# Kernel tuning notes

Measured on AMD Instinct MI355X. Metric: run time of the kernel, lower is better.

Reference implementation:

```python
import jax, jax.numpy as jnp
import numpy as np

V, H, NH, I, L, P = 32000, 1024, 16, 4096, 8, 2048
B, S = 2, 2048
DH = H // NH
EPS = 1e-5


def setup_inputs() -> dict:
    key = jax.random.key(0)
    ks = jax.random.split(key, 12)
    std = 0.02
    inp = {
        'input_ids': jax.random.randint(ks[0], (B, S), 0, V),
        'attention_mask': jnp.ones((B, S), dtype=jnp.float32),
        'tok_emb': jax.random.normal(ks[1], (V, H), jnp.float32) * std,
        'pos_emb': jax.random.normal(ks[2], (P, H), jnp.float32) * std,
        # per-layer params stacked on leading L dim (torch Linear convention: y = x @ W.T + b)
        'Wq': jax.random.normal(ks[3], (L, H, H), jnp.float32) * std,
        'bq': jnp.zeros((L, H), jnp.float32),
        'Wk': jax.random.normal(ks[4], (L, H, H), jnp.float32) * std,
        'bk': jnp.zeros((L, H), jnp.float32),
        'Wv': jax.random.normal(ks[5], (L, H, H), jnp.float32) * std,
        'bv': jnp.zeros((L, H), jnp.float32),
        'Wi': jax.random.normal(ks[6], (L, I, H), jnp.float32) * std,
        'bi': jnp.zeros((L, I), jnp.float32),
        'Wo': jax.random.normal(ks[7], (L, H, I), jnp.float32) * std,
        'bo': jnp.zeros((L, H), jnp.float32),
        'ln1_g': jnp.ones((L, H), jnp.float32),
        'ln1_b': jnp.zeros((L, H), jnp.float32),
        'ln2_g': jnp.ones((L, H), jnp.float32),
        'ln2_b': jnp.zeros((L, H), jnp.float32),
        'lnf_g': jnp.ones((H,), jnp.float32),
        'lnf_b': jnp.zeros((H,), jnp.float32),
        'Wlm': jax.random.normal(ks[8], (V, H), jnp.float32) * std,
    }
    return inp


def _layer_norm(x, g, b):
    m = jnp.mean(x, axis=-1, keepdims=True)
    v = jnp.var(x, axis=-1, keepdims=True)
    return (x - m) * jax.lax.rsqrt(v + EPS) * g + b


def reference(input_ids, attention_mask, tok_emb, pos_emb, Wq, bq, Wk, bk, Wv, bv,
              Wi, bi, Wo, bo, ln1_g, ln1_b, ln2_g, ln2_b, lnf_g, lnf_b, Wlm):
    b, s = input_ids.shape
    h = tok_emb[input_ids] + pos_emb[jnp.arange(s)][None, :, :]  # [B,S,H]
    mask = (1.0 - attention_mask)[:, None, None, :] * -10000.0   # [B,1,1,S]
    scale = 1.0 / (DH ** 0.5)

    def split_heads(x):  # [B,S,H] -> [B,NH,S,DH]
        return x.reshape(b, s, NH, DH).transpose(0, 2, 1, 3)

    def block(h, p):
        wq, bq_, wk, bk_, wv, bv_, wi, bi_, wo, bo_, g1, b1, g2, b2 = p
        q = split_heads(h @ wq.T + bq_)
        k = split_heads(h @ wk.T + bk_)
        v = split_heads(h @ wv.T + bv_)
        scores = jnp.einsum('bhqd,bhkd->bhqk', q, k) * scale + mask
        probs = jax.nn.softmax(scores, axis=-1)
        ctx = jnp.einsum('bhqk,bhkd->bhqd', probs, v)
        ctx = ctx.transpose(0, 2, 1, 3).reshape(b, s, H)
        h1 = _layer_norm(h + ctx, g1, b1)
        mlp = jax.nn.gelu(h1 @ wi.T + bi_, approximate=False) @ wo.T + bo_
        return _layer_norm(h1 + mlp, g2, b2), None

    h, _ = jax.lax.scan(block, h, (Wq, bq, Wk, bk, Wv, bv, Wi, bi, Wo, bo,
                                   ln1_g, ln1_b, ln2_g, ln2_b))
    h = _layer_norm(h, lnf_g, lnf_b)
    return h @ Wlm.T  # [B,S,V]
```

## Files before the change

### kernel.cpp

```cpp
#include <hip/hip_runtime.h>
#include <hip/hip_bf16.h>

#define V_ 32000
#define H_ 1024
#define NH_ 16
#define I_ 4096
#define L_ 8
#define B_ 2
#define S_ 2048
#define DH_ 64
#define M_ 4096
#define QS_ 3072
#define NSP_ 2

typedef __attribute__((ext_vector_type(4))) float f32x4;
typedef __attribute__((ext_vector_type(8))) short s16x8;

#define BARRIER() do { asm volatile("" ::: "memory"); __builtin_amdgcn_s_barrier(); asm volatile("" ::: "memory"); } while (0)
#define SCHEDB()  __builtin_amdgcn_sched_barrier(0)

__device__ __forceinline__ unsigned short f2b(float f) {
  union { float f; unsigned u; } x; x.f = f;
  return (unsigned short)((x.u + 0x7FFFu + ((x.u >> 16) & 1u)) >> 16);
}

__device__ __forceinline__ void gl_lds16(const unsigned short* g, unsigned short* l) {
  __builtin_amdgcn_global_load_lds(
      (__attribute__((address_space(1))) const void*)g,
      (__attribute__((address_space(3))) void*)l, 16, 0, 0);
}

__global__ __launch_bounds__(256) void wcvt(const float* __restrict__ src,
                                            unsigned short* __restrict__ dst) {
  size_t i = ((size_t)blockIdx.x * 256 + threadIdx.x) * 4;
  float4 v = *(const float4*)(src + i);
  ushort4 b;
  b.x = f2b(v.x); b.y = f2b(v.y); b.z = f2b(v.z); b.w = f2b(v.w);
  *(ushort4*)(dst + i) = b;
}

__global__ __launch_bounds__(256) void qkvcat_all(const float* __restrict__ q,
                                                  const float* __restrict__ k,
                                                  const float* __restrict__ v,
                                                  unsigned short* __restrict__ dst) {
  size_t i = ((size_t)blockIdx.x * 256 + threadIdx.x) * 4;
  size_t l = i / (3u * H_ * H_);
  size_t r = i - l * (3u * H_ * H_);
  const float* s; size_t off;
  if (r < (size_t)H_ * H_)          { s = q; off = l * H_ * H_ + r; }
  else if (r < 2u * H_ * H_)        { s = k; off = l * H_ * H_ + r - (size_t)H_ * H_; }
  else                              { s = v; off = l * H_ * H_ + r - 2u * H_ * H_; }
  float4 vv = *(const float4*)(s + off);
  ushort4 b;
  b.x = f2b(vv.x); b.y = f2b(vv.y); b.z = f2b(vv.z); b.w = f2b(vv.w);
  *(ushort4*)(dst + i) = b;
}

__global__ __launch_bounds__(256) void qkvcat(const float* __restrict__ q,
                                              const float* __restrict__ k,
                                              const float* __restrict__ v,
                                              unsigned short* __restrict__ dst) {
  int i = (blockIdx.x * 256 + threadIdx.x) * 4;
  const float* s; int off;
  if (i < H_ * H_)          { s = q; off = i; }
  else if (i < 2 * H_ * H_) { s = k; off = i - H_ * H_; }
  else                      { s = v; off = i - 2 * H_ * H_; }
  float4 vv = *(const float4*)(s + off);
  ushort4 b;
  b.x = f2b(vv.x); b.y = f2b(vv.y); b.z = f2b(vv.z); b.w = f2b(vv.w);
  *(ushort4*)(dst + i) = b;
}

__global__ __launch_bounds__(256) void bcat(const float* __restrict__ bq,
                                            const float* __restrict__ bk,
                                            const float* __restrict__ bv,
                                            float* __restrict__ dst) {
  int i = blockIdx.x * 256 + threadIdx.x;
  int l = i / (3 * H_), r = i - l * 3 * H_;
  int p = r >> 10, c = r & (H_ - 1);
  const float* s = (p == 0) ? bq : ((p == 1) ? bk : bv);
  dst[i] = s[l * H_ + c];
}

__global__ __launch_bounds__(256) void embed_kernel(
    const int* __restrict__ ids, const float* __restrict__ tok,
    const float* __restrict__ pos, float* __restrict__ h,
    unsigned short* __restrict__ xbf)
{
  int row = blockIdx.x;
  int c4 = threadIdx.x;
  int id = ids[row];
  int s = row & (S_ - 1);
  float4 tv = ((const float4*)(tok + (size_t)id * H_))[c4];
  float4 pv = ((const float4*)(pos + (size_t)s * H_))[c4];
  float4 v; v.x = tv.x + pv.x; v.y = tv.y + pv.y; v.z = tv.z + pv.z; v.w = tv.w + pv.w;
  ((float4*)(h + (size_t)row * H_))[c4] = v;
  ushort4 b; b.x = f2b(v.x); b.y = f2b(v.y); b.z = f2b(v.z); b.w = f2b(v.w);
  ((ushort4*)(xbf + (size_t)row * H_))[c4] = b;
}

template<int EPI>
__global__ __launch_bounds__(256) void gemm_bt(
    const unsigned short* __restrict__ A, const unsigned short* __restrict__ Wb,
    const float* __restrict__ bias, float* __restrict__ outf,
    unsigned short* __restrict__ outb, unsigned short* __restrict__ vt,
    int M, int N, int K, int ksz)
{
  __shared__ unsigned short As[2][128][32];
  __shared__ unsigned short Bs[2][128][32];
  int t = threadIdx.x;
  int lane = t & 63, wid = t >> 6;
  int m0 = blockIdx.x * 128, n0 = blockIdx.y * 128;
  int z = blockIdx.z;
  int koff = z * ksz;
  const float* bz = (z == 0) ? bias : nullptr;
  if (EPI == 0) outf += (size_t)z * M * N;
  int wm = (wid >> 1) * 64, wn = (wid & 1) * 64;
  int fr = lane & 15, hi = lane >> 4;
  int lrow = lane >> 2;
  int lcolsw = (((lane & 3) ^ (lrow & 3)) * 8);
  int ke = ((hi ^ (fr & 3)) * 8);

  f32x4 acc[4][4] = {};

  const unsigned short* Abase = A  + (size_t)(m0 + wid * 32 + lrow) * K + lcolsw;
  const unsigned short* Bbase = Wb + (size_t)(n0 + wid * 32 + lrow) * K + lcolsw;

  auto stage = [&](int s, int k0) {
    gl_lds16(Abase + k0,                  &As[s][wid * 32][0]);
    gl_lds16(Abase + k0 + (size_t)16 * K, &As[s][wid * 32 + 16][0]);
    gl_lds16(Bbase + k0,                  &Bs[s][wid * 32][0]);
    gl_lds16(Bbase + k0 + (size_t)16 * K, &Bs[s][wid * 32 + 16][0]);
  };

  stage(0, koff);

  int cur = 0;
  for (int k0 = koff; k0 < koff + ksz; k0 += 32) {
    asm volatile("s_waitcnt vmcnt(0)" ::: "memory");
    BARRIER();
    if (k0 + 32 < koff + ksz) stage(cur ^ 1, k0 + 32);
    SCHEDB();
    s16x8 af[4], bfr[4];
    #pragma unroll
    for (int i = 0; i < 4; ++i) af[i]  = *(const s16x8*)(&As[cur][wm + i * 16 + fr][ke]);
    #pragma unroll
    for (int j = 0; j < 4; ++j) bfr[j] = *(const s16x8*)(&Bs[cur][wn + j * 16 + fr][ke]);
    #pragma unroll
    for (int i = 0; i < 4; ++i)
      #pragma unroll
      for (int j = 0; j < 4; ++j)
        acc[i][j] = __builtin_amdgcn_mfma_f32_16x16x32_bf16(af[i], bfr[j], acc[i][j], 0, 0, 0);
    cur ^= 1;
  }

  int fq = lane >> 4;
  if (EPI == 3) {
    #pragma unroll
    for (int i = 0; i < 4; ++i) {
      #pragma unroll
      for (int j = 0; j < 4; ++j) {
        int col = n0 + wn + j * 16 + fr;
        int row0_ = m0 + wm + i * 16 + fq * 4;
        float bcol = bz ? bz[col] : 0.f;
        if (col < 2 * H_) {
          #pragma unroll
          for (int r = 0; r < 4; ++r)
            outb[(size_t)(row0_ + r) * N + col] = f2b(acc[i][j][r] + bcol);
        } else {
          int d = col - 2 * H_;
          int bh = (row0_ >> 11) * NH_ + (d >> 6);
          int s0 = row0_ & (S_ - 1);
          ushort4 pk;
          pk.x = f2b(acc[i][j][0] + bcol);
          pk.y = f2b(acc[i][j][1] + bcol);
          pk.z = f2b(acc[i][j][2] + bcol);
          pk.w = f2b(acc[i][j][3] + bcol);
          *(ushort4*)(vt + ((size_t)bh * DH_ + (d & 63)) * S_ + s0) = pk;
        }
      }
    }
    return;
  }
  #pragma unroll
  for (int i = 0; i < 4; ++i) {
    #pragma unroll
    for (int j = 0; j < 4; ++j) {
      #pragma unroll
      for (int r = 0; r < 4; ++r) {
        int row = m0 + wm + i * 16 + fq * 4 + r;
        int col = n0 + wn + j * 16 + fr;
        float v = acc[i][j][r] + (bz ? bz[col] : 0.f);
        if (EPI == 0) {
          outf[(size_t)row * N + col] = v;
        } else if (EPI == 1) {
          float ge = 0.5f * v * (1.0f + erff(v * 0.70710678118f));
          outb[(size_t)row * N + col] = f2b(ge);
        } else {
          outb[(size_t)row * N + col] = f2b(v);
        }
      }
    }
  }
}

template<int EPI>
__global__ __launch_bounds__(512, 2) void gemm256(
    const unsigned short* __restrict__ A, const unsigned short* __restrict__ Wb,
    const float* __restrict__ bias, float* __restrict__ outf,
    unsigned short* __restrict__ outb, int M, int N, int K)
{
  __shared__ unsigned short ASm[2][16384];
  __shared__ unsigned short BSm[2][16384];

  const int t = threadIdx.x;
  const int lane = t & 63, wid = t >> 6;
  const int wm = wid >> 2, wn = wid & 3;
  const int fr = lane & 15, hi = lane >> 4;

  const int Nt = N >> 8;
  const int nwg = gridDim.x;
  const int cpx = nwg >> 3;
  int bid = (int)blockIdx.x;
  int swz = (bid & 7) * cpx + (bid >> 3);
  int band = swz / (4 * Nt);
  int rem = swz - band * (4 * Nt);
  const int m0 = (band * 4 + (rem & 3)) << 8;
  const int n0 = (rem >> 2) << 8;

  const int NT = K >> 6;

  const int srow = lane >> 3;
  const int scol = ((lane & 7) ^ srow) << 3;
  const int ch0 = wid * 2;

  const int axorb = (fr & 7) << 4;
  const int koe0 = ((hi * 16) ^ axorb) >> 1;
  const int koe1 = (((hi * 16) | 64) ^ axorb) >> 1;

  f32x4 acc[8][4] = {};

  auto stage_half = [&](int slot, int h, int k0) {
    if (h < 2) {
      const unsigned short* src =
          A + (size_t)(m0 + h * 128 + ch0 * 8 + srow) * K + k0 + scol;
      unsigned short* dst = &ASm[slot][(h * 128 + ch0 * 8) * 64];
      gl_lds16(src, dst);
      gl_lds16(src + (size_t)8 * K, dst + 8 * 64);
    } else {
      const unsigned short* src =
          Wb + (size_t)(n0 + (h - 2) * 128 + ch0 * 8 + srow) * K + k0 + scol;
      unsigned short* dst = &BSm[slot][((h - 2) * 128 + ch0 * 8) * 64];
      gl_lds16(src, dst);
      gl_lds16(src + (size_t)8 * K, dst + 8 * 64);
    }
  };

  stage_half(0, 2, 0); stage_half(0, 3, 0); stage_half(0, 0, 0); stage_half(0, 1, 0);

  s16x8 af0[4][2], af1[4][2], bfv[4][2];

  for (int T = 0; T < NT; ++T) {
    const int s = T & 1;
    const int k1 = (T + 1) << 6;
    const bool more = (T + 1 < NT);

    asm volatile("s_waitcnt vmcnt(0)" ::: "memory");
    BARRIER();

    const unsigned short* As_ = ASm[s];
    const unsigned short* Bs_ = BSm[s];

    #pragma unroll
    for (int mi = 0; mi < 4; ++mi) {
      const unsigned short* p = As_ + (wm * 128 + mi * 16 + fr) * 64;
      af0[mi][0] = *(const s16x8*)(p + koe0);
      af0[mi][1] = *(const s16x8*)(p + koe1);
    }
    #pragma unroll
    for (int nj = 0; nj < 4; ++nj) {
      const unsigned short* p = Bs_ + (wn * 64 + nj * 16 + fr) * 64;
      bfv[nj][0] = *(const s16x8*)(p + koe0);
      bfv[nj][1] = *(const s16x8*)(p + koe1);
    }
    if (more) stage_half(s ^ 1, 2, k1);
    SCHEDB();
    __builtin_amdgcn_s_setprio(1);
    #pragma unroll
    for (int mi = 0; mi < 4; ++mi)
      #pragma unroll
      for (int nj = 0; nj < 2; ++nj) {
        acc[mi][nj] = __builtin_amdgcn_mfma_f32_16x16x32_bf16(af0[mi][0], bfv[nj][0], acc[mi][nj], 0, 0, 0);
        acc[mi][nj] = __builtin_amdgcn_mfma_f32_16x16x32_bf16(af0[mi][1], bfv[nj][1], acc[mi][nj], 0, 0, 0);
      }
    __builtin_amdgcn_s_setprio(0);
    SCHEDB();

    #pragma unroll
    for (int mi = 0; mi < 4; ++mi) {
      const unsigned short* p = As_ + (wm * 128 + (mi + 4) * 16 + fr) * 64;
      af1[mi][0] = *(const s16x8*)(p + koe0);
      af1[mi][1] = *(const s16x8*)(p + koe1);
    }
    if (more) stage_half(s ^ 1, 3, k1);
    SCHEDB();
    __builtin_amdgcn_s_setprio(1);
    #pragma unroll
    for (int mi = 0; mi < 4; ++mi)
      #pragma unroll
      for (int nj = 2; nj < 4; ++nj) {
        acc[mi][nj] = __builtin_amdgcn_mfma_f32_16x16x32_bf16(af0[mi][0], bfv[nj][0], acc[mi][nj], 0, 0, 0);
        acc[mi][nj] = __builtin_amdgcn_mfma_f32_16x16x32_bf16(af0[mi][1], bfv[nj][1], acc[mi][nj], 0, 0, 0);
      }
    __builtin_amdgcn_s_setprio(0);
    SCHEDB();

    if (more) stage_half(s ^ 1, 0, k1);
    SCHEDB();
    __builtin_amdgcn_s_setprio(1);
    #pragma unroll
    for (int mi = 0; mi < 4; ++mi)
      #pragma unroll
      for (int nj = 2; nj < 4; ++nj) {
        acc[mi + 4][nj] = __builtin_amdgcn_mfma_f32_16x16x32_bf16(af1[mi][0], bfv[nj][0], acc[mi + 4][nj], 0, 0, 0);
        acc[mi + 4][nj] = __builtin_amdgcn_mfma_f32_16x16x32_bf16(af1[mi][1], bfv[nj][1], acc[mi + 4][nj], 0, 0, 0);
      }
    __builtin_amdgcn_s_setprio(0);
    SCHEDB();

    if (more) stage_half(s ^ 1, 1, k1);
    SCHEDB();
    __builtin_amdgcn_s_setprio(1);
    #pragma unroll
    for (int mi = 0; mi < 4; ++mi)
      #pragma unroll
      for (int nj = 0; nj < 2; ++nj) {
        acc[mi + 4][nj] = __builtin_amdgcn_mfma_f32_16x16x32_bf16(af1[mi][0], bfv[nj][0], acc[mi + 4][nj], 0, 0, 0);
        acc[mi + 4][nj] = __builtin_amdgcn_mfma_f32_16x16x32_bf16(af1[mi][1], bfv[nj][1], acc[mi + 4][nj], 0, 0, 0);
      }
    __builtin_amdgcn_s_setprio(0);
  }

  #pragma unroll
  for (int mi = 0; mi < 8; ++mi) {
    #pragma unroll
    for (int nj = 0; nj < 4; ++nj) {
      #pragma unroll
      for (int r = 0; r < 4; ++r) {
        int row = m0 + wm * 128 + mi * 16 + hi * 4 + r;
        int col = n0 + wn * 64 + nj * 16 + fr;
        float v = acc[mi][nj][r] + (bias ? bias[col] : 0.f);
        if (EPI == 0) {
          outf[(size_t)row * N + col] = v;
        } else if (EPI == 1) {
          float ge = 0.5f * v * (1.0f + erff(v * 0.70710678118f));
          outb[(size_t)row * N + col] = f2b(ge);
        } else {
          outb[(size_t)row * N + col] = f2b(v);
        }
      }
    }
  }
}

#define KB_ 64
#define SPL_ 1024
__global__ __launch_bounds__(512, 2) void flash_mfma(
    const unsigned short* __restrict__ qb,
    const unsigned short* __restrict__ kb,
    const unsigned short* __restrict__ vtb,
    const float* __restrict__ mask,
    float* __restrict__ opart,
    float2* __restrict__ ml)
{
  __shared__ unsigned short K2[2][KB_ * DH_];
  __shared__ unsigned short V2[2][DH_ * KB_];
  __shared__ unsigned short Ps[8][16][72];
  __shared__ float xpose[8][16];

  const float LOG2E = 1.4426950408889634f;
  const float SCL = 0.125f * LOG2E;
  int t = threadIdx.x, lane = t & 63, wid = t >> 6;
  int blk = blockIdx.x;
  int bh = blk & 31;
  int rest = blk >> 5;
  int qt = rest & 15, sp = rest >> 4;
  int b = bh >> 4, hh = bh & 15;
  int row0 = b * S_ + qt * 128 + wid * 16;
  int fr = lane & 15, hi = lane >> 4;
  const float* mrow = mask + (size_t)b * S_;
  const int kv0 = sp * SPL_;

  s16x8 qf[2];
  {
    const unsigned short* qrow = qb + (size_t)(row0 + fr) * QS_ + hh * DH_;
    qf[0] = *(const s16x8*)(qrow + hi * 8);
    qf[1] = *(const s16x8*)(qrow + 32 + hi * 8);
  }

  float m_run = -3.0e38f, l_run = 0.f;
  f32x4 octx[4] = {};

  const unsigned short* Kbase = kb + (size_t)b * S_ * QS_ + hh * DH_;
  const unsigned short* Vbase = vtb + (size_t)bh * DH_ * S_;

  int crow = lane >> 3;
  int scol = ((lane & 7) ^ crow) * 8;

  auto stage = [&](int slot, int t0) {
    gl_lds16(Kbase + (size_t)(t0 + wid * 8 + crow) * QS_ + scol, &K2[slot][wid * 512]);
    gl_lds16(Vbase + (size_t)(wid * 8 + crow) * S_ + t0 + scol,  &V2[slot][wid * 512]);
  };

  stage(0, kv0);

  const int swz = (fr & 7) * 8;

  int tt = 0;
  for (int t0 = kv0; t0 < kv0 + SPL_; t0 += KB_, ++tt) {
    int slot = tt & 1;
    __syncthreads();
    if (t0 + KB_ < kv0 + SPL_) stage(slot ^ 1, t0 + KB_);

    f32x4 sacc[4] = {};
    #pragma unroll
    for (int g = 0; g < 4; ++g) {
      #pragma unroll
      for (int i = 0; i < 2; ++i) {
        s16x8 kf = *(const s16x8*)(&K2[slot][(g * 16 + fr) * 64 + ((i * 32 + hi * 8) ^ swz)]);
        sacc[g] = __builtin_amdgcn_mfma_f32_16x16x32_bf16(kf, qf[i], sacc[g], 0, 0, 0);
      }
    }

    float tm = -3.0e38f;
    #pragma unroll
    for (int g = 0; g < 4; ++g) {
      float4 mq = *(const float4*)(mrow + t0 + g * 16 + hi * 4);
      #pragma unroll
      for (int r = 0; r < 4; ++r) {
        float mk = (1.0f - ((const float*)&mq)[r]) * (-10000.0f * LOG2E);
        float v = sacc[g][r] * SCL + mk;
        sacc[g][r] = v;
        tm = fmaxf(tm, v);
      }
    }
    tm = fmaxf(tm, __shfl_xor(tm, 16));
    tm = fmaxf(tm, __shfl_xor(tm, 32));

    if (!__all(tm <= m_run + 8.0f)) {
      float mn = fmaxf(m_run, tm);
      float corr = exp2f(m_run - mn);
      m_run = mn; l_run *= corr;
      xpose[wid][fr] = corr;
      float cr0 = xpose[wid][hi * 4 + 0];
      float cr1 = xpose[wid][hi * 4 + 1];
      float cr2 = xpose[wid][hi * 4 + 2];
      float cr3 = xpose[wid][hi * 4 + 3];
      #pragma unroll
      for (int dg = 0; dg < 4; ++dg) {
        octx[dg][0] *= cr0; octx[dg][1] *= cr1;
        octx[dg][2] *= cr2; octx[dg][3] *= cr3;
      }
    }

    float ps = 0.f;
    #pragma unroll
    for (int g = 0; g < 4; ++g) {
      float p0 = exp2f(sacc[g][0] - m_run);
      float p1 = exp2f(sacc[g][1] - m_run);
      float p2 = exp2f(sacc[g][2] - m_run);
      float p3 = exp2f(sacc[g][3] - m_run);
      ps += (p0 + p1) + (p2 + p3);
      uint2 pk;
      pk.x = (unsigned)f2b(p0) | ((unsigned)f2b(p1) << 16);
      pk.y = (unsigned)f2b(p2) | ((unsigned)f2b(p3) << 16);
      *(uint2*)(&Ps[wid][fr][g * 16 + hi * 4]) = pk;
    }
    ps += __shfl_xor(ps, 16);
    ps += __shfl_xor(ps, 32);
    l_run += ps;

    #pragma unroll
    for (int kc = 0; kc < 2; ++kc) {
      s16x8 pf = *(const s16x8*)(&Ps[wid][fr][kc * 32 + hi * 8]);
      #pragma unroll
      for (int dg = 0; dg < 4; ++dg) {
        s16x8 vf2 = *(const s16x8*)(&V2[slot][(dg * 16 + fr) * 64 + ((kc * 32 + hi * 8) ^ swz)]);
        octx[dg] = __builtin_amdgcn_mfma_f32_16x16x32_bf16(pf, vf2, octx[dg], 0, 0, 0);
      }
    }
  }

  float* ob = opart + (size_t)sp * M_ * H_;
  #pragma unroll
  for (int dg = 0; dg < 4; ++dg) {
    size_t base = (size_t)(row0 + hi * 4) * H_ + hh * DH_ + dg * 16 + fr;
    ob[base]          = octx[dg][0];
    ob[base + H_]     = octx[dg][1];
    ob[base + 2 * H_] = octx[dg][2];
    ob[base + 3 * H_] = octx[dg][3];
  }
  if (hi == 0)
    ml[((size_t)sp * 32 + bh) * S_ + qt * 128 + wid * 16 + fr] =
        make_float2(m_run, l_run);
}

__global__ __launch_bounds__(256) void add_ln_mrg(
    const float* __restrict__ x, const float* __restrict__ o0,
    const float* __restrict__ o1, const float2* __restrict__ ml,
    const float* __restrict__ g, const float* __restrict__ bb,
    float* __restrict__ outf, unsigned short* __restrict__ outb)
{
  __shared__ float a1[4], a2[4];
  int row = blockIdx.x, t = threadIdx.x;
  int hh = t >> 4;
  int bh = (row >> 11) * NH_ + hh;
  int q = row & (S_ - 1);
  float2 a = ml[(size_t)bh * S_ + q];
  float2 c = ml[(size_t)(32 + bh) * S_ + q];
  float m = fmaxf(a.x, c.x);
  float w0 = exp2f(a.x - m), w1 = exp2f(c.x - m);
  float inv0 = 1.0f / (a.y * w0 + c.y * w1);
  float4 v  = ((const float4*)(x  + (size_t)row * H_))[t];
  float4 u0 = ((const float4*)(o0 + (size_t)row * H_))[t];
  float4 u1 = ((const float4*)(o1 + (size_t)row * H_))[t];
  v.x += (u0.x * w0 + u1.x * w1) * inv0;
  v.y += (u0.y * w0 + u1.y * w1) * inv0;
  v.z += (u0.z * w0 + u1.z * w1) * inv0;
  v.w += (u0.w * w0 + u1.w * w1) * inv0;
  float s1 = v.x + v.y + v.z + v.w;
  float s2 = v.x * v.x + v.y * v.y + v.z * v.z + v.w * v.w;
  #pragma unroll
  for (int d = 32; d; d >>= 1) { s1 += __shfl_xor(s1, d); s2 += __shfl_xor(s2, d); }
  if ((t & 63) == 0) { a1[t >> 6] = s1; a2[t >> 6] = s2; }
  __syncthreads();
  s1 = a1[0] + a1[1] + a1[2] + a1[3];
  s2 = a2[0] + a2[1] + a2[2] + a2[3];
  float mean = s1 * (1.0f / H_);
  float var = s2 * (1.0f / H_) - mean * mean;
  float inv = rsqrtf(var + 1e-5f);
  float4 gv = ((const float4*)g)[t];
  float4 bv = ((const float4*)bb)[t];
  float4 o;
  o.x = (v.x - mean) * inv * gv.x + bv.x;
  o.y = (v.y - mean) * inv * gv.y + bv.y;
  o.z = (v.z - mean) * inv * gv.z + bv.z;
  o.w = (v.w - mean) * inv * gv.w + bv.w;
  if (outf) ((float4*)(outf + (size_t)row * H_))[t] = o;
  if (outb) {
    ushort4 ob; ob.x = f2b(o.x); ob.y = f2b(o.y); ob.z = f2b(o.z); ob.w = f2b(o.w);
    ((ushort4*)(outb + (size_t)row * H_))[t] = ob;
  }
}

__global__ __launch_bounds__(256) void add_ln(
    const float* __restrict__ x, const float* __restrict__ y,
    const float* __restrict__ y2,
    const float* __restrict__ g, const float* __restrict__ bb,
    float* __restrict__ outf, unsigned short* __restrict__ outb)
{
  __shared__ float a1[4], a2[4];
  int row = blockIdx.x, t = threadIdx.x;
  float4 v = ((const float4*)(x + (size_t)row * H_))[t];
  if (y) {
    float4 u = ((const float4*)(y + (size_t)row * H_))[t];
    v.x += u.x; v.y += u.y; v.z += u.z; v.w += u.w;
  }
  if (y2) {
    float4 u = ((const float4*)(y2 + (size_t)row * H_))[t];
    v.x += u.x; v.y += u.y; v.z += u.z; v.w += u.w;
  }
  float s1 = v.x + v.y + v.z + v.w;
  float s2 = v.x * v.x + v.y * v.y + v.z * v.z + v.w * v.w;
  #pragma unroll
  for (int d = 32; d; d >>= 1) { s1 += __shfl_xor(s1, d); s2 += __shfl_xor(s2, d); }
  if ((t & 63) == 0) { a1[t >> 6] = s1; a2[t >> 6] = s2; }
  __syncthreads();
  s1 = a1[0] + a1[1] + a1[2] + a1[3];
  s2 = a2[0] + a2[1] + a2[2] + a2[3];
  float mean = s1 * (1.0f / H_);
  float var = s2 * (1.0f / H_) - mean * mean;
  float inv = rsqrtf(var + 1e-5f);
  float4 gv = ((const float4*)g)[t];
  float4 bv = ((const float4*)bb)[t];
  float4 o;
  o.x = (v.x - mean) * inv * gv.x + bv.x;
  o.y = (v.y - mean) * inv * gv.y + bv.y;
  o.z = (v.z - mean) * inv * gv.z + bv.z;
  o.w = (v.w - mean) * inv * gv.w + bv.w;
  if (outf) ((float4*)(outf + (size_t)row * H_))[t] = o;
  if (outb) {
    ushort4 ob; ob.x = f2b(o.x); ob.y = f2b(o.y); ob.z = f2b(o.z); ob.w = f2b(o.w);
    ((ushort4*)(outb + (size_t)row * H_))[t] = ob;
  }
}

extern "C" void kernel_launch(void* const* d_in, const int* in_sizes, int n_in,
                              void* d_out, int out_size, void* d_ws, size_t ws_size,
                              hipStream_t stream) {
  const int*   ids  = (const int*)d_in[0];
  const float* mask = (const float*)d_in[1];
  const float* tok  = (const float*)d_in[2];
  const float* pos  = (const float*)d_in[3];
  const float* Wq   = (const float*)d_in[4];
  const float* bq   = (const float*)d_in[5];
  const float* Wk   = (const float*)d_in[6];
  const float* bk   = (const float*)d_in[7];
  const float* Wv   = (const float*)d_in[8];
  const float* bv   = (const float*)d_in[9];
  const float* Wi   = (const float*)d_in[10];
  const float* bi   = (const float*)d_in[11];
  const float* Wo   = (const float*)d_in[12];
  const float* bo   = (const float*)d_in[13];
  const float* ln1g = (const float*)d_in[14];
  const float* ln1b = (const float*)d_in[15];
  const float* ln2g = (const float*)d_in[16];
  const float* ln2b = (const float*)d_in[17];
  const float* lnfg = (const float*)d_in[18];
  const float* lnfb = (const float*)d_in[19];
  const float* Wlm  = (const float*)d_in[20];
  float* out = (float*)d_out;

  char* w = (char*)d_ws;
  size_t off = 0;
  auto alloc = [&](size_t bytes) { void* p = w + off; off = (off + bytes + 255) & ~(size_t)255; return p; };
  float* h     = (float*)alloc((size_t)M_ * H_ * 4);
  unsigned short* qkvb  = (unsigned short*)alloc((size_t)M_ * QS_ * 2);
  unsigned short* vtb   = (unsigned short*)alloc((size_t)B_ * NH_ * DH_ * S_ * 2);
  unsigned short* xbf   = (unsigned short*)alloc((size_t)M_ * H_ * 2);
  unsigned short* midbf = (unsigned short*)alloc((size_t)M_ * I_ * 2);
  float* bqkv  = (float*)alloc((size_t)L_ * QS_ * 4);
  float* opart = (float*)alloc((size_t)NSP_ * M_ * H_ * 4);
  float2* mlbuf = (float2*)alloc((size_t)NSP_ * 32 * S_ * 8);

  size_t wqkv_b = (size_t)L_ * 3 * H_ * H_ * 2;
  size_t wi_bb  = (size_t)L_ * I_ * H_ * 2;
  size_t wo_bb  = (size_t)L_ * H_ * I_ * 2;
  size_t wlm_bb = (size_t)V_ * H_ * 2;
  bool big = (ws_size - off) >= (wqkv_b + wi_bb + wo_bb + wlm_bb + 4 * 256);

  unsigned short *wqkv, *wi_a, *wo_a, *wlm_a, *wbuf = nullptr;
  if (big) {
    wqkv  = (unsigned short*)alloc(wqkv_b);
    wi_a  = (unsigned short*)alloc(wi_bb);
    wo_a  = (unsigned short*)alloc(wo_bb);
    wlm_a = (unsigned short*)alloc(wlm_bb);
    qkvcat_all<<<dim3((unsigned)((size_t)L_ * 3 * H_ * H_ / 1024)), 256, 0, stream>>>(Wq, Wk, Wv, wqkv);
    wcvt<<<dim3((unsigned)((size_t)L_ * I_ * H_ / 1024)), 256, 0, stream>>>(Wi, wi_a);
    wcvt<<<dim3((unsigned)((size_t)L_ * H_ * I_ / 1024)), 256, 0, stream>>>(Wo, wo_a);
    wcvt<<<dim3((unsigned)((size_t)V_ * H_ / 1024)), 256, 0, stream>>>(Wlm, wlm_a);
  } else {
    wbuf = (unsigned short*)alloc((size_t)V_ * H_ * 2);
  }

  bcat<<<dim3(L_ * QS_ / 256), 256, 0, stream>>>(bq, bk, bv, bqkv);
  embed_kernel<<<dim3(M_), 256, 0, stream>>>(ids, tok, pos, h, xbf);

  for (int l = 0; l < L_; ++l) {
    const unsigned short* wq_l;
    if (big) wq_l = wqkv + (size_t)l * 3 * H_ * H_;
    else {
      qkvcat<<<dim3(3 * H_ * H_ / 1024), 256, 0, stream>>>(
          Wq + (size_t)l * H_ * H_, Wk + (size_t)l * H_ * H_, Wv + (size_t)l * H_ * H_, wbuf);
      wq_l = wbuf;
    }
    gemm_bt<3><<<dim3(M_ / 128, QS_ / 128, 1), 256, 0, stream>>>(
        xbf, wq_l, bqkv + (size_t)l * QS_, nullptr, qkvb, vtb, M_, QS_, H_, H_);

    flash_mfma<<<dim3(B_ * NH_ * S_ / 128 * NSP_), 512, 0, stream>>>(
        qkvb, qkvb + H_, vtb, mask, opart, mlbuf);

    add_ln_mrg<<<dim3(M_), 256, 0, stream>>>(
        h, opart, opart + (size_t)M_ * H_, mlbuf,
        ln1g + l * H_, ln1b + l * H_, h, xbf);

    const unsigned short* wi_l;
    if (big) wi_l = wi_a + (size_t)l * I_ * H_;
    else {
      wcvt<<<dim3(I_ * H_ / 1024), 256, 0, stream>>>(Wi + (size_t)l * I_ * H_, wbuf);
      wi_l = wbuf;
    }
    gemm256<1><<<dim3((M_ / 256) * (I_ / 256)), 512, 0, stream>>>(
        xbf, wi_l, bi + l * I_, nullptr, midbf, M_, I_, H_);

    const unsigned short* wo_l;
    if (big) wo_l = wo_a + (size_t)l * H_ * I_;
    else {
      wcvt<<<dim3(H_ * I_ / 1024), 256, 0, stream>>>(Wo + (size_t)l * H_ * I_, wbuf);
      wo_l = wbuf;
    }
    gemm_bt<0><<<dim3(M_ / 128, H_ / 128, 2), 256, 0, stream>>>(
        midbf, wo_l, bo + l * H_, opart, nullptr, nullptr, M_, H_, I_, I_ / 2);

    add_ln<<<dim3(M_), 256, 0, stream>>>(
        h, opart, opart + (size_t)M_ * H_,
        ln2g + l * H_, ln2b + l * H_, h, xbf);
  }

  add_ln<<<dim3(M_), 256, 0, stream>>>(h, nullptr, nullptr, lnfg, lnfb, nullptr, xbf);
  const unsigned short* wlm_l;
  if (big) wlm_l = wlm_a;
  else {
    wcvt<<<dim3(V_ * H_ / 1024), 256, 0, stream>>>(Wlm, wbuf);
    wlm_l = wbuf;
  }
  gemm256<0><<<dim3((M_ / 256) * (V_ / 256)), 512, 0, stream>>>(
      xbf, wlm_l, nullptr, out, nullptr, M_, V_, H_);
}
```

Baseline: 2.853 ms.

## Software-pipeline flash attention so QK of next tile overlaps PV of previous

Restructures the flash attention inner loop into QK, softmax and PV stages, and skews them so that tile i's QK MFMAs are issued alongside tile i-1's PV MFMAs. V staging gets a third LDS buffer so V of the previous tile stays resident while the next loads. The launch bounds drop the minimum-two-blocks-per-SM hint to give the compiler more registers for the extra live state (sacc, packed probabilities). This risks lower occupancy and higher register pressure in exchange for better MFMA/VALU overlap.

After: 2.878 ms. About the same (+0.9%).

```diff
diff --git a/kernel.cpp b/kernel.cpp
--- a/kernel.cpp
+++ b/kernel.cpp
@@ -365,7 +365,8 @@
 
 #define KB_ 64
 #define SPL_ 1024
-__global__ __launch_bounds__(512, 2) void flash_mfma(
+#define NTT_ (SPL_ / KB_)
+__global__ __launch_bounds__(512) void flash_mfma(
     const unsigned short* __restrict__ qb,
     const unsigned short* __restrict__ kb,
     const unsigned short* __restrict__ vtb,
@@ -374,7 +375,7 @@
     float2* __restrict__ ml)
 {
   __shared__ unsigned short K2[2][KB_ * DH_];
-  __shared__ unsigned short V2[2][DH_ * KB_];
+  __shared__ unsigned short V2[3][DH_ * KB_];
   __shared__ unsigned short Ps[8][16][72];
   __shared__ float xpose[8][16];
 
@@ -400,6 +401,8 @@
 
   float m_run = -3.0e38f, l_run = 0.f;
   f32x4 octx[4] = {};
+  f32x4 sacc[4];
+  uint2 pp[4];
 
   const unsigned short* Kbase = kb + (size_t)b * S_ * QS_ + hh * DH_;
   const unsigned short* Vbase = vtb + (size_t)bh * DH_ * S_;
@@ -407,31 +410,26 @@
   int crow = lane >> 3;
   int scol = ((lane & 7) ^ crow) * 8;
 
-  auto stage = [&](int slot, int t0) {
-    gl_lds16(Kbase + (size_t)(t0 + wid * 8 + crow) * QS_ + scol, &K2[slot][wid * 512]);
-    gl_lds16(Vbase + (size_t)(wid * 8 + crow) * S_ + t0 + scol,  &V2[slot][wid * 512]);
+  auto stageKV = [&](int ks, int vs, int t0) {
+    gl_lds16(Kbase + (size_t)(t0 + wid * 8 + crow) * QS_ + scol, &K2[ks][wid * 512]);
+    gl_lds16(Vbase + (size_t)(wid * 8 + crow) * S_ + t0 + scol,  &V2[vs][wid * 512]);
   };
 
-  stage(0, kv0);
-
   const int swz = (fr & 7) * 8;
 
-  int tt = 0;
-  for (int t0 = kv0; t0 < kv0 + SPL_; t0 += KB_, ++tt) {
-    int slot = tt & 1;
-    __syncthreads();
-    if (t0 + KB_ < kv0 + SPL_) stage(slot ^ 1, t0 + KB_);
-
-    f32x4 sacc[4] = {};
+  auto QK = [&](int ks) {
     #pragma unroll
     for (int g = 0; g < 4; ++g) {
+      sacc[g] = f32x4{0.f, 0.f, 0.f, 0.f};
       #pragma unroll
       for (int i = 0; i < 2; ++i) {
-        s16x8 kf = *(const s16x8*)(&K2[slot][(g * 16 + fr) * 64 + ((i * 32 + hi * 8) ^ swz)]);
+        s16x8 kf = *(const s16x8*)(&K2[ks][(g * 16 + fr) * 64 + ((i * 32 + hi * 8) ^ swz)]);
         sacc[g] = __builtin_amdgcn_mfma_f32_16x16x32_bf16(kf, qf[i], sacc[g], 0, 0, 0);
       }
     }
-
+  };
+
+  auto SM = [&](int t0) {
     float tm = -3.0e38f;
     #pragma unroll
     for (int g = 0; g < 4; ++g) {
@@ -471,25 +469,43 @@
       float p2 = exp2f(sacc[g][2] - m_run);
       float p3 = exp2f(sacc[g][3] - m_run);
       ps += (p0 + p1) + (p2 + p3);
-      uint2 pk;
-      pk.x = (unsigned)f2b(p0) | ((unsigned)f2b(p1) << 16);
-      pk.y = (unsigned)f2b(p2) | ((unsigned)f2b(p3) << 16);
-      *(uint2*)(&Ps[wid][fr][g * 16 + hi * 4]) = pk;
+      pp[g].x = (unsigned)f2b(p0) | ((unsigned)f2b(p1) << 16);
+      pp[g].y = (unsigned)f2b(p2) | ((unsigned)f2b(p3) << 16);
     }
     ps += __shfl_xor(ps, 16);
     ps += __shfl_xor(ps, 32);
     l_run += ps;
-
+  };
+
+  auto PV = [&](int vs) {
+    #pragma unroll
+    for (int g = 0; g < 4; ++g)
+      *(uint2*)(&Ps[wid][fr][g * 16 + hi * 4]) = pp[g];
     #pragma unroll
     for (int kc = 0; kc < 2; ++kc) {
       s16x8 pf = *(const s16x8*)(&Ps[wid][fr][kc * 32 + hi * 8]);
       #pragma unroll
       for (int dg = 0; dg < 4; ++dg) {
-        s16x8 vf2 = *(const s16x8*)(&V2[slot][(dg * 16 + fr) * 64 + ((kc * 32 + hi * 8) ^ swz)]);
+        s16x8 vf2 = *(const s16x8*)(&V2[vs][(dg * 16 + fr) * 64 + ((kc * 32 + hi * 8) ^ swz)]);
         octx[dg] = __builtin_amdgcn_mfma_f32_16x16x32_bf16(pf, vf2, octx[dg], 0, 0, 0);
       }
     }
-  }
+  };
+
+  stageKV(0, 0, kv0);
+  __syncthreads();
+  if (NTT_ > 1) stageKV(1, 1, kv0 + KB_);
+  QK(0);
+  SM(kv0);
+
+  for (int i = 1; i < NTT_; ++i) {
+    __syncthreads();
+    if (i + 1 < NTT_) stageKV((i + 1) & 1, (i + 1) % 3, kv0 + (i + 1) * KB_);
+    QK(i & 1);
+    PV((i - 1) % 3);
+    SM(kv0 + i * KB_);
+  }
+  PV((NTT_ - 1) % 3);
 
   float* ob = opart + (size_t)sp * M_ * H_;
   #pragma unroll
```
